# Kernel tuning notes

Measured on AMD Instinct MI355X. Metric: run time of the kernel, lower is better.

The kernel has to match this reference:

```python
import jax, jax.numpy as jnp
import numpy as np

WS = 7          # window size (square)
NUM_HEADS = 4
DIM = 128
B_ = 16384
NW = 64         # number of distinct shift masks


def _relative_coords(ws):
    # [N, N, 2] normalized relative coordinates, N = ws*ws
    ch = jnp.arange(ws, dtype=jnp.float32)
    cw = jnp.arange(ws, dtype=jnp.float32)
    coords = jnp.stack(jnp.meshgrid(ch, cw, indexing='ij'))          # [2, ws, ws]
    flat = coords.reshape(2, -1)                                      # [2, N]
    rel = flat[:, :, None] - flat[:, None, :]                         # [2, N, N]
    rel = jnp.transpose(rel, (1, 2, 0))                               # [N, N, 2]
    denom = jnp.array([max(ws - 1, 1), max(ws - 1, 1)], jnp.float32)
    return rel / denom


def setup_inputs() -> dict:
    key = jax.random.key(0)
    ks = jax.random.split(key, 8)
    N = WS * WS
    return {
        'x': jax.random.normal(ks[0], (B_, N, DIM), jnp.float32),
        'mask': jax.random.normal(ks[1], (NW, N, N), jnp.float32),
        'qkv_w': jax.random.normal(ks[2], (DIM, 3 * DIM), jnp.float32) * 0.02,
        'qkv_b': jnp.zeros((3 * DIM,), jnp.float32),
        'mlp_w1': jax.random.normal(ks[3], (2, 64), jnp.float32) * 0.5,
        'mlp_b1': jnp.zeros((64,), jnp.float32),
        'mlp_w2': jax.random.normal(ks[4], (64, NUM_HEADS), jnp.float32) * 0.1,
        'mlp_b2': jnp.zeros((NUM_HEADS,), jnp.float32),
        'proj_w': jax.random.normal(ks[5], (DIM, DIM), jnp.float32) * 0.02,
        'proj_b': jnp.zeros((DIM,), jnp.float32),
    }


def reference(x, mask, qkv_w, qkv_b, mlp_w1, mlp_b1, mlp_w2, mlp_b2, proj_w, proj_b):
    B, N, C = x.shape
    H = NUM_HEADS
    hd = C // H
    scale = hd ** (-0.5)

    qkv = (x @ qkv_w + qkv_b).reshape(B, N, 3, H, hd)
    qkv = jnp.transpose(qkv, (2, 0, 3, 1, 4))          # [3, B, H, N, hd]
    q, k, v = qkv[0] * scale, qkv[1], qkv[2]

    attn = jnp.einsum('bhnd,bhmd->bhnm', q, k)          # [B, H, N, N]

    # MLP-derived relative position bias (exact-erf GELU, as torch nn.GELU default)
    rel = _relative_coords(WS)                          # [N, N, 2]
    hmid = jax.nn.gelu(rel @ mlp_w1 + mlp_b1, approximate=False)
    bias = hmid @ mlp_w2 + mlp_b2                       # [N, N, H]
    bias = jnp.transpose(bias, (2, 0, 1))               # [H, N, N]
    attn = attn + bias[None]

    nW = mask.shape[0]
    attn = attn.reshape(B // nW, nW, H, N, N) + mask[None, :, None]
    attn = attn.reshape(B, H, N, N)
    attn = jax.nn.softmax(attn, axis=-1)

    out = jnp.einsum('bhnm,bhmd->bhnd', attn, v)        # [B, H, N, hd]
    out = jnp.transpose(out, (0, 2, 1, 3)).reshape(B, N, C)
    return out @ proj_w + proj_b
```

## Files before the change

### kernel.cpp

```cpp
#include <hip/hip_runtime.h>
#include <hip/hip_bf16.h>
#include <math.h>

typedef __bf16 bf16_t;
typedef __bf16 bf16x4 __attribute__((ext_vector_type(4)));
typedef __bf16 bf16x8 __attribute__((ext_vector_type(8)));
typedef float  f32x4  __attribute__((ext_vector_type(4)));

#define QKV_SCALE 0.17677669529663687f

#define WS_QKVWT   0u
#define WS_PROJWT  98304u
#define WS_QKVB    131072u
#define WS_MASKP   135168u
#define WS_BIAST   1183744u

__global__ __launch_bounds__(256) void prep_kernel(
    const float* __restrict__ mask,
    const float* __restrict__ qkv_w, const float* __restrict__ qkv_b,
    const float* __restrict__ mlp_w1, const float* __restrict__ mlp_b1,
    const float* __restrict__ mlp_w2, const float* __restrict__ mlp_b2,
    const float* __restrict__ proj_w,
    bf16_t* __restrict__ qkv_wT, bf16_t* __restrict__ proj_wT,
    float* __restrict__ qkv_bs, float* __restrict__ mask_pad,
    float* __restrict__ bias_t)
{
    const int blk = blockIdx.x;
    const int tid = threadIdx.x;
    if (blk < 1024) {
        const int idx = blk * 256 + tid;
        const int wi = idx >> 12, cell = idx & 4095;
        const int q = cell >> 6, kk = cell & 63;
        float val;
        if (q < 49 && kk < 49)      val = mask[wi * 2401 + q * 49 + kk];
        else if (kk >= 49)          val = -3.0e38f;
        else                        val = 0.0f;
        mask_pad[idx] = val;
    } else if (blk < 1040) {
        const int cell = (blk - 1024) * 256 + tid;
        const int q = cell >> 6, kk = cell & 63;
        float b0 = 0.f, b1 = 0.f, b2 = 0.f, b3 = 0.f;
        if (q < 49 && kk < 49) {
            const float dy = (float)(q / 7 - kk / 7) * (1.0f / 6.0f);
            const float dx = (float)(q % 7 - kk % 7) * (1.0f / 6.0f);
            b0 = mlp_b2[0]; b1 = mlp_b2[1]; b2 = mlp_b2[2]; b3 = mlp_b2[3];
            for (int j = 0; j < 64; ++j) {
                const float pre = dy * mlp_w1[j] + dx * mlp_w1[64 + j] + mlp_b1[j];
                const float g = 0.5f * pre * (1.0f + erff(pre * 0.70710678118654752f));
                b0 += g * mlp_w2[j * 4 + 0];
                b1 += g * mlp_w2[j * 4 + 1];
                b2 += g * mlp_w2[j * 4 + 2];
                b3 += g * mlp_w2[j * 4 + 3];
            }
        }
        bias_t[0 * 4096 + cell] = b0;
        bias_t[1 * 4096 + cell] = b1;
        bias_t[2 * 4096 + cell] = b2;
        bias_t[3 * 4096 + cell] = b3;
    } else if (blk < 1232) {
        const int idx = (blk - 1040) * 256 + tid;
        const int n = idx >> 7, k = idx & 127;
        float v = qkv_w[k * 384 + n];
        if (n < 128) v *= QKV_SCALE;
        qkv_wT[idx] = (bf16_t)v;
    } else if (blk < 1296) {
        const int idx = (blk - 1232) * 256 + tid;
        const int n = idx >> 7, k = idx & 127;
        proj_wT[idx] = (bf16_t)proj_w[k * 128 + n];
    } else {
        if (tid < 384) {
            float v = qkv_b[tid];
            if (tid < 128) v *= QKV_SCALE;
            qkv_bs[tid] = v;
        }
    }
}

__global__ __launch_bounds__(512, 4) void swin_main_kernel(
    const float* __restrict__ x,
    const bf16_t* __restrict__ qkv_wT,
    const bf16_t* __restrict__ proj_wT,
    const float* __restrict__ qkv_bs,
    const float* __restrict__ proj_b,
    const float* __restrict__ mask_pad,
    const float* __restrict__ bias_t,
    float* __restrict__ out)
{
    __shared__ __align__(16) unsigned char smem[65536];
    const int QB = 16384, KBo = 32768, VT = 49152;

    const int win  = blockIdx.x;
    const int tid  = threadIdx.x;
    const int wv   = tid >> 6;
    const int a    = wv >> 1;
    const int b2   = wv & 1;
    const int lane = tid & 63;
    const int c16  = lane & 15;
    const int q4   = lane >> 4;
    const int swz  = (c16 & 7) << 4;
    const f32x4 zf = {0.f, 0.f, 0.f, 0.f};

    {
        const float* xg = x + (size_t)win * 6272;
#pragma unroll
        for (int cc = 0; cc < 2; ++cc) {
            const int c   = tid + 512 * cc;
            const int row = c >> 4;
            const int k8  = (c & 15) << 3;
            const int off = ((row << 8) + (k8 << 1)) ^ ((row & 7) << 4);
            bf16x8 v;
            if (row < 49) {
                const float4 a0 = *(const float4*)(xg + row * 128 + k8);
                const float4 a1 = *(const float4*)(xg + row * 128 + k8 + 4);
                v[0] = (bf16_t)a0.x; v[1] = (bf16_t)a0.y;
                v[2] = (bf16_t)a0.z; v[3] = (bf16_t)a0.w;
                v[4] = (bf16_t)a1.x; v[5] = (bf16_t)a1.y;
                v[6] = (bf16_t)a1.z; v[7] = (bf16_t)a1.w;
            } else {
#pragma unroll
                for (int j = 0; j < 8; ++j) v[j] = (bf16_t)0.0f;
            }
            *(bf16x8*)&smem[off] = v;
        }
    }
    __syncthreads();

    int trow[2];
    trow[0] = (16 * (2 * b2 + 0) + c16) << 8;
    trow[1] = (16 * (2 * b2 + 1) + c16) << 8;

    f32x4 qk[4][2];
#pragma unroll
    for (int m = 0; m < 4; ++m) { qk[m][0] = zf; qk[m][1] = zf; }
#pragma unroll
    for (int ks = 0; ks < 4; ++ks) {
        bf16x8 xf[2];
#pragma unroll
        for (int nt = 0; nt < 2; ++nt)
            xf[nt] = *(const bf16x8*)&smem[(trow[nt] + 64 * ks + 16 * q4) ^ swz];
#pragma unroll
        for (int m = 0; m < 4; ++m) {
            const int t = 4 * a + m;
            const bf16x8 wf = *(const bf16x8*)(qkv_wT + (16 * t + c16) * 128 + ks * 32 + q4 * 8);
#pragma unroll
            for (int nt = 0; nt < 2; ++nt)
                qk[m][nt] = __builtin_amdgcn_mfma_f32_16x16x32_bf16(wf, xf[nt], qk[m][nt], 0, 0, 0);
        }
    }
#pragma unroll
    for (int m = 0; m < 4; ++m) {
        const int t = 4 * a + m;
        const float4 bi = *(const float4*)(qkv_bs + 16 * t + 4 * q4);
        const int base = (t < 8) ? QB : KBo;
        const int dimb = (t < 8) ? (32 * t + 8 * q4) : (32 * (t - 8) + 8 * q4);
#pragma unroll
        for (int nt = 0; nt < 2; ++nt) {
            bf16x4 pk;
            pk[0] = (bf16_t)(qk[m][nt][0] + bi.x); pk[1] = (bf16_t)(qk[m][nt][1] + bi.y);
            pk[2] = (bf16_t)(qk[m][nt][2] + bi.z); pk[3] = (bf16_t)(qk[m][nt][3] + bi.w);
            *(bf16x4*)&smem[base + ((trow[nt] + dimb) ^ swz)] = pk;
        }
    }

    f32x4 va[2][2];
#pragma unroll
    for (int mv = 0; mv < 2; ++mv) { va[mv][0] = zf; va[mv][1] = zf; }
#pragma unroll
    for (int ks = 0; ks < 4; ++ks) {
        bf16x8 xf[2];
#pragma unroll
        for (int nt = 0; nt < 2; ++nt)
            xf[nt] = *(const bf16x8*)&smem[(trow[nt] + 64 * ks + 16 * q4) ^ swz];
#pragma unroll
        for (int mv = 0; mv < 2; ++mv) {
            const int vc = 16 * (2 * a + mv) + c16;
            const bf16x8 vf = *(const bf16x8*)(qkv_wT + (256 + vc) * 128 + ks * 32 + q4 * 8);
#pragma unroll
            for (int nt = 0; nt < 2; ++nt)
                va[mv][nt] = __builtin_amdgcn_mfma_f32_16x16x32_bf16(xf[nt], vf, va[mv][nt], 0, 0, 0);
        }
    }
#pragma unroll
    for (int mv = 0; mv < 2; ++mv) {
        const int vc = 16 * (2 * a + mv) + c16;
        const float qv = qkv_bs[256 + vc];
#pragma unroll
        for (int nt = 0; nt < 2; ++nt) {
            const int slot2 = (32 * b2 + 8 * q4 + 4 * nt) << 1;
            bf16x4 pk;
            pk[0] = (bf16_t)(va[mv][nt][0] + qv); pk[1] = (bf16_t)(va[mv][nt][1] + qv);
            pk[2] = (bf16_t)(va[mv][nt][2] + qv); pk[3] = (bf16_t)(va[mv][nt][3] + qv);
            *(bf16x4*)&smem[VT + (((vc << 7) + slot2) ^ swz)] = pk;
        }
    }
    __syncthreads();

    bf16x8 Qf[2];
#pragma unroll
    for (int nt = 0; nt < 2; ++nt)
        Qf[nt] = *(const bf16x8*)&smem[QB + ((trow[nt] + 64 * a + 16 * q4) ^ swz)];
    f32x4 st[4][2];
#pragma unroll
    for (int mtk = 0; mtk < 4; ++mtk) {
        const bf16x8 Kf = *(const bf16x8*)&smem[KBo + ((((16 * mtk + c16) << 8) + 64 * a + 16 * q4) ^ swz)];
        st[mtk][0] = __builtin_amdgcn_mfma_f32_16x16x32_bf16(Kf, Qf[0], zf, 0, 0, 0);
        st[mtk][1] = __builtin_amdgcn_mfma_f32_16x16x32_bf16(Kf, Qf[1], zf, 0, 0, 0);
    }

    const float* mp = mask_pad + ((size_t)(win & 63) << 12);
    const float* bt = bias_t + (a << 12);
    bf16x8 Pf[2][2];
#pragma unroll
    for (int ntq = 0; ntq < 2; ++ntq) {
        const int qtok = 16 * (2 * b2 + ntq) + c16;
        float mx = -3.0e38f;
#pragma unroll
        for (int mtk = 0; mtk < 4; ++mtk) {
            const float4 mv4 = *(const float4*)(mp + qtok * 64 + 16 * mtk + 4 * q4);
            const float4 bv4 = *(const float4*)(bt + qtok * 64 + 16 * mtk + 4 * q4);
            st[mtk][ntq][0] += mv4.x + bv4.x; st[mtk][ntq][1] += mv4.y + bv4.y;
            st[mtk][ntq][2] += mv4.z + bv4.z; st[mtk][ntq][3] += mv4.w + bv4.w;
#pragma unroll
            for (int r = 0; r < 4; ++r) mx = fmaxf(mx, st[mtk][ntq][r]);
        }
        mx = fmaxf(mx, __shfl_xor(mx, 16));
        mx = fmaxf(mx, __shfl_xor(mx, 32));
        float sm = 0.0f;
#pragma unroll
        for (int mtk = 0; mtk < 4; ++mtk)
#pragma unroll
            for (int r = 0; r < 4; ++r) {
                const float p = __expf(st[mtk][ntq][r] - mx);
                st[mtk][ntq][r] = p;
                sm += p;
            }
        sm += __shfl_xor(sm, 16);
        sm += __shfl_xor(sm, 32);
        const float rp = 1.0f / sm;
#pragma unroll
        for (int ksv = 0; ksv < 2; ++ksv)
#pragma unroll
            for (int r = 0; r < 4; ++r) {
                Pf[ntq][ksv][r]     = (bf16_t)(st[2 * ksv][ntq][r] * rp);
                Pf[ntq][ksv][4 + r] = (bf16_t)(st[2 * ksv + 1][ntq][r] * rp);
            }
    }

    f32x4 ot[2][2];
#pragma unroll
    for (int mtd = 0; mtd < 2; ++mtd) { ot[mtd][0] = zf; ot[mtd][1] = zf; }
#pragma unroll
    for (int ksv = 0; ksv < 2; ++ksv)
#pragma unroll
        for (int mtd = 0; mtd < 2; ++mtd) {
            const bf16x8 av = *(const bf16x8*)&smem[VT + ((((32 * a + 16 * mtd + c16) << 7) + 64 * ksv + 16 * q4) ^ swz)];
#pragma unroll
            for (int ntq = 0; ntq < 2; ++ntq)
                ot[mtd][ntq] = __builtin_amdgcn_mfma_f32_16x16x32_bf16(av, Pf[ntq][ksv], ot[mtd][ntq], 0, 0, 0);
        }

#pragma unroll
    for (int mtd = 0; mtd < 2; ++mtd)
#pragma unroll
        for (int ntq = 0; ntq < 2; ++ntq) {
            bf16x4 pk;
#pragma unroll
            for (int r = 0; r < 4; ++r) pk[r] = (bf16_t)ot[mtd][ntq][r];
            *(bf16x4*)&smem[(trow[ntq] + ((32 * a + 16 * mtd + 4 * q4) << 1)) ^ swz] = pk;
        }
    __syncthreads();

    const int oc_il = 32 * a + 8 * (c16 >> 2) + (c16 & 3);
    f32x4 pj[2][2];
#pragma unroll
    for (int mt = 0; mt < 2; ++mt) { pj[mt][0] = zf; pj[mt][1] = zf; }
#pragma unroll
    for (int ks = 0; ks < 4; ++ks) {
        const bf16x8 aw0 = *(const bf16x8*)(proj_wT + (oc_il + 0) * 128 + ks * 32 + q4 * 8);
        const bf16x8 aw1 = *(const bf16x8*)(proj_wT + (oc_il + 4) * 128 + ks * 32 + q4 * 8);
#pragma unroll
        for (int ntq = 0; ntq < 2; ++ntq) {
            const bf16x8 bo = *(const bf16x8*)&smem[(trow[ntq] + 64 * ks + 16 * q4) ^ swz];
            pj[0][ntq] = __builtin_amdgcn_mfma_f32_16x16x32_bf16(aw0, bo, pj[0][ntq], 0, 0, 0);
            pj[1][ntq] = __builtin_amdgcn_mfma_f32_16x16x32_bf16(aw1, bo, pj[1][ntq], 0, 0, 0);
        }
    }

    {
        float* og = out + (size_t)win * 6272;
        const int oc0 = 32 * a + 8 * q4;
        const float4 pb0 = *(const float4*)(proj_b + oc0);
        const float4 pb1 = *(const float4*)(proj_b + oc0 + 4);
#pragma unroll
        for (int ntq = 0; ntq < 2; ++ntq) {
            const int tok = 16 * (2 * b2 + ntq) + c16;
            if (tok < 49) {
                float4 v0, v1;
                v0.x = pj[0][ntq][0] + pb0.x; v0.y = pj[0][ntq][1] + pb0.y;
                v0.z = pj[0][ntq][2] + pb0.z; v0.w = pj[0][ntq][3] + pb0.w;
                v1.x = pj[1][ntq][0] + pb1.x; v1.y = pj[1][ntq][1] + pb1.y;
                v1.z = pj[1][ntq][2] + pb1.z; v1.w = pj[1][ntq][3] + pb1.w;
                *(float4*)(og + tok * 128 + oc0)     = v0;
                *(float4*)(og + tok * 128 + oc0 + 4) = v1;
            }
        }
    }
}

extern "C" void kernel_launch(void* const* d_in, const int* in_sizes, int n_in,
                              void* d_out, int out_size, void* d_ws, size_t ws_size,
                              hipStream_t stream) {
    const float* x      = (const float*)d_in[0];
    const float* mask   = (const float*)d_in[1];
    const float* qkv_w  = (const float*)d_in[2];
    const float* qkv_b  = (const float*)d_in[3];
    const float* mlp_w1 = (const float*)d_in[4];
    const float* mlp_b1 = (const float*)d_in[5];
    const float* mlp_w2 = (const float*)d_in[6];
    const float* mlp_b2 = (const float*)d_in[7];
    const float* proj_w = (const float*)d_in[8];
    const float* proj_b = (const float*)d_in[9];
    float* out = (float*)d_out;

    unsigned char* ws = (unsigned char*)d_ws;
    bf16_t* qkv_wT   = (bf16_t*)(ws + WS_QKVWT);
    bf16_t* proj_wT  = (bf16_t*)(ws + WS_PROJWT);
    float*  qkv_bs   = (float*)(ws + WS_QKVB);
    float*  mask_pad = (float*)(ws + WS_MASKP);
    float*  bias_t   = (float*)(ws + WS_BIAST);

    hipLaunchKernelGGL(prep_kernel, dim3(1297), dim3(256), 0, stream,
                       mask, qkv_w, qkv_b, mlp_w1, mlp_b1, mlp_w2, mlp_b2, proj_w,
                       qkv_wT, proj_wT, qkv_bs, mask_pad, bias_t);
    hipLaunchKernelGGL(swin_main_kernel, dim3(16384), dim3(512), 0, stream,
                       x, qkv_wT, proj_wT, qkv_bs, proj_b, mask_pad, bias_t, out);
}
```

Before: 795.8 us.

## Process eight windows per block with double-buffered x prefetch

Each block now loops over several consecutive windows instead of one. While the current window is computed, the next window's x tile is loaded from global memory into registers and written into a second LDS buffer, which overlaps load latency with compute. Per-block constants such as biases are hoisted out of the loop. In exchange, LDS use grows to 80KB, occupancy drops to 2 blocks, the grid shrinks by 8x, and an extra barrier is added per window.

```diff
diff --git a/kernel.cpp b/kernel.cpp
--- a/kernel.cpp
+++ b/kernel.cpp
@@ -8,6 +8,7 @@
 typedef float  f32x4  __attribute__((ext_vector_type(4)));
 
 #define QKV_SCALE 0.17677669529663687f
+#define NWIN 8
 
 #define WS_QKVWT   0u
 #define WS_PROJWT  98304u
@@ -76,7 +77,7 @@
     }
 }
 
-__global__ __launch_bounds__(512, 4) void swin_main_kernel(
+__global__ __launch_bounds__(512, 2) void swin_main_kernel(
     const float* __restrict__ x,
     const bf16_t* __restrict__ qkv_wT,
     const bf16_t* __restrict__ proj_wT,
@@ -86,10 +87,9 @@
     const float* __restrict__ bias_t,
     float* __restrict__ out)
 {
-    __shared__ __align__(16) unsigned char smem[65536];
-    const int QB = 16384, KBo = 32768, VT = 49152;
-
-    const int win  = blockIdx.x;
+    __shared__ __align__(16) unsigned char smem[81920];
+    const int QB = 32768, KBo = 49152, VT = 65536;
+
     const int tid  = threadIdx.x;
     const int wv   = tid >> 6;
     const int a    = wv >> 1;
@@ -98,20 +98,43 @@
     const int c16  = lane & 15;
     const int q4   = lane >> 4;
     const int swz  = (c16 & 7) << 4;
+    const int wbase = blockIdx.x * NWIN;
     const f32x4 zf = {0.f, 0.f, 0.f, 0.f};
 
+    float4 biQK[4];
+#pragma unroll
+    for (int m = 0; m < 4; ++m)
+        biQK[m] = *(const float4*)(qkv_bs + 16 * (4 * a + m) + 4 * q4);
+    float qv[2];
+    qv[0] = qkv_bs[256 + 16 * (2 * a + 0) + c16];
+    qv[1] = qkv_bs[256 + 16 * (2 * a + 1) + c16];
+    const int oc_il = 32 * a + 8 * (c16 >> 2) + (c16 & 3);
+    const int oc0   = 32 * a + 8 * q4;
+    const float4 pb0 = *(const float4*)(proj_b + oc0);
+    const float4 pb1 = *(const float4*)(proj_b + oc0 + 4);
+    const float* bt = bias_t + (a << 12);
+
+    int trow[2];
+    trow[0] = (16 * (2 * b2 + 0) + c16) << 8;
+    trow[1] = (16 * (2 * b2 + 1) + c16) << 8;
+
+    int srow[2], sk8[2], soff[2];
+#pragma unroll
+    for (int cc = 0; cc < 2; ++cc) {
+        const int c = tid + 512 * cc;
+        srow[cc] = c >> 4;
+        sk8[cc]  = (c & 15) << 3;
+        soff[cc] = ((srow[cc] << 8) + (sk8[cc] << 1)) ^ ((srow[cc] & 7) << 4);
+    }
+
     {
-        const float* xg = x + (size_t)win * 6272;
+        const float* xg = x + (size_t)wbase * 6272;
 #pragma unroll
         for (int cc = 0; cc < 2; ++cc) {
-            const int c   = tid + 512 * cc;
-            const int row = c >> 4;
-            const int k8  = (c & 15) << 3;
-            const int off = ((row << 8) + (k8 << 1)) ^ ((row & 7) << 4);
             bf16x8 v;
-            if (row < 49) {
-                const float4 a0 = *(const float4*)(xg + row * 128 + k8);
-                const float4 a1 = *(const float4*)(xg + row * 128 + k8 + 4);
+            if (srow[cc] < 49) {
+                const float4 a0 = *(const float4*)(xg + srow[cc] * 128 + sk8[cc]);
+                const float4 a1 = *(const float4*)(xg + srow[cc] * 128 + sk8[cc] + 4);
                 v[0] = (bf16_t)a0.x; v[1] = (bf16_t)a0.y;
                 v[2] = (bf16_t)a0.z; v[3] = (bf16_t)a0.w;
                 v[4] = (bf16_t)a1.x; v[5] = (bf16_t)a1.y;
@@ -120,190 +143,216 @@
 #pragma unroll
                 for (int j = 0; j < 8; ++j) v[j] = (bf16_t)0.0f;
             }
-            *(bf16x8*)&smem[off] = v;
+            *(bf16x8*)&smem[soff[cc]] = v;
         }
     }
     __syncthreads();
 
-    int trow[2];
-    trow[0] = (16 * (2 * b2 + 0) + c16) << 8;
-    trow[1] = (16 * (2 * b2 + 1) + c16) << 8;
-
-    f32x4 qk[4][2];
-#pragma unroll
-    for (int m = 0; m < 4; ++m) { qk[m][0] = zf; qk[m][1] = zf; }
-#pragma unroll
-    for (int ks = 0; ks < 4; ++ks) {
-        bf16x8 xf[2];
-#pragma unroll
-        for (int nt = 0; nt < 2; ++nt)
-            xf[nt] = *(const bf16x8*)&smem[(trow[nt] + 64 * ks + 16 * q4) ^ swz];
+    for (int i = 0; i < NWIN; ++i) {
+        const int win  = wbase + i;
+        const int xcur = (i & 1) << 14;
+        const int xnxt = ((i & 1) ^ 1) << 14;
+        const bool pf  = (i + 1 < NWIN);
+
+        float4 pa[2][2];
+        if (pf) {
+            const float* xn = x + (size_t)(win + 1) * 6272;
+#pragma unroll
+            for (int cc = 0; cc < 2; ++cc) {
+                if (srow[cc] < 49) {
+                    pa[cc][0] = *(const float4*)(xn + srow[cc] * 128 + sk8[cc]);
+                    pa[cc][1] = *(const float4*)(xn + srow[cc] * 128 + sk8[cc] + 4);
+                }
+            }
+        }
+
+        f32x4 qk[4][2];
+#pragma unroll
+        for (int m = 0; m < 4; ++m) { qk[m][0] = zf; qk[m][1] = zf; }
+#pragma unroll
+        for (int ks = 0; ks < 4; ++ks) {
+            bf16x8 xf[2];
+#pragma unroll
+            for (int nt = 0; nt < 2; ++nt)
+                xf[nt] = *(const bf16x8*)&smem[xcur + ((trow[nt] + 64 * ks + 16 * q4) ^ swz)];
+#pragma unroll
+            for (int m = 0; m < 4; ++m) {
+                const int t = 4 * a + m;
+                const bf16x8 wf = *(const bf16x8*)(qkv_wT + (16 * t + c16) * 128 + ks * 32 + q4 * 8);
+#pragma unroll
+                for (int nt = 0; nt < 2; ++nt)
+                    qk[m][nt] = __builtin_amdgcn_mfma_f32_16x16x32_bf16(wf, xf[nt], qk[m][nt], 0, 0, 0);
+            }
+        }
 #pragma unroll
         for (int m = 0; m < 4; ++m) {
             const int t = 4 * a + m;
-            const bf16x8 wf = *(const bf16x8*)(qkv_wT + (16 * t + c16) * 128 + ks * 32 + q4 * 8);
+            const int base = (t < 8) ? QB : KBo;
+            const int dimb = (t < 8) ? (32 * t + 8 * q4) : (32 * (t - 8) + 8 * q4);
+#pragma unroll
+            for (int nt = 0; nt < 2; ++nt) {
+                bf16x4 pk;
+                pk[0] = (bf16_t)(qk[m][nt][0] + biQK[m].x); pk[1] = (bf16_t)(qk[m][nt][1] + biQK[m].y);
+                pk[2] = (bf16_t)(qk[m][nt][2] + biQK[m].z); pk[3] = (bf16_t)(qk[m][nt][3] + biQK[m].w);
+                *(bf16x4*)&smem[base + ((trow[nt] + dimb) ^ swz)] = pk;
+            }
+        }
+
+        f32x4 va[2][2];
+#pragma unroll
+        for (int mv = 0; mv < 2; ++mv) { va[mv][0] = zf; va[mv][1] = zf; }
+#pragma unroll
+        for (int ks = 0; ks < 4; ++ks) {
+            bf16x8 xf[2];
 #pragma unroll
             for (int nt = 0; nt < 2; ++nt)
-                qk[m][nt] = __builtin_amdgcn_mfma_f32_16x16x32_bf16(wf, xf[nt], qk[m][nt], 0, 0, 0);
-        }
-    }
-#pragma unroll
-    for (int m = 0; m < 4; ++m) {
-        const int t = 4 * a + m;
-        const float4 bi = *(const float4*)(qkv_bs + 16 * t + 4 * q4);
-        const int base = (t < 8) ? QB : KBo;
-        const int dimb = (t < 8) ? (32 * t + 8 * q4) : (32 * (t - 8) + 8 * q4);
-#pragma unroll
-        for (int nt = 0; nt < 2; ++nt) {
-            bf16x4 pk;
-            pk[0] = (bf16_t)(qk[m][nt][0] + bi.x); pk[1] = (bf16_t)(qk[m][nt][1] + bi.y);
-            pk[2] = (bf16_t)(qk[m][nt][2] + bi.z); pk[3] = (bf16_t)(qk[m][nt][3] + bi.w);
-            *(bf16x4*)&smem[base + ((trow[nt] + dimb) ^ swz)] = pk;
-        }
-    }
-
-    f32x4 va[2][2];
-#pragma unroll
-    for (int mv = 0; mv < 2; ++mv) { va[mv][0] = zf; va[mv][1] = zf; }
-#pragma unroll
-    for (int ks = 0; ks < 4; ++ks) {
-        bf16x8 xf[2];
-#pragma unroll
-        for (int nt = 0; nt < 2; ++nt)
-            xf[nt] = *(const bf16x8*)&smem[(trow[nt] + 64 * ks + 16 * q4) ^ swz];
+                xf[nt] = *(const bf16x8*)&smem[xcur + ((trow[nt] + 64 * ks + 16 * q4) ^ swz)];
+#pragma unroll
+            for (int mv = 0; mv < 2; ++mv) {
+                const int vc = 16 * (2 * a + mv) + c16;
+                const bf16x8 vf = *(const bf16x8*)(qkv_wT + (256 + vc) * 128 + ks * 32 + q4 * 8);
+#pragma unroll
+                for (int nt = 0; nt < 2; ++nt)
+                    va[mv][nt] = __builtin_amdgcn_mfma_f32_16x16x32_bf16(xf[nt], vf, va[mv][nt], 0, 0, 0);
+            }
+        }
 #pragma unroll
         for (int mv = 0; mv < 2; ++mv) {
             const int vc = 16 * (2 * a + mv) + c16;
-            const bf16x8 vf = *(const bf16x8*)(qkv_wT + (256 + vc) * 128 + ks * 32 + q4 * 8);
-#pragma unroll
-            for (int nt = 0; nt < 2; ++nt)
-                va[mv][nt] = __builtin_amdgcn_mfma_f32_16x16x32_bf16(xf[nt], vf, va[mv][nt], 0, 0, 0);
-        }
-    }
-#pragma unroll
-    for (int mv = 0; mv < 2; ++mv) {
-        const int vc = 16 * (2 * a + mv) + c16;
-        const float qv = qkv_bs[256 + vc];
-#pragma unroll
-        for (int nt = 0; nt < 2; ++nt) {
-            const int slot2 = (32 * b2 + 8 * q4 + 4 * nt) << 1;
-            bf16x4 pk;
-            pk[0] = (bf16_t)(va[mv][nt][0] + qv); pk[1] = (bf16_t)(va[mv][nt][1] + qv);
-            pk[2] = (bf16_t)(va[mv][nt][2] + qv); pk[3] = (bf16_t)(va[mv][nt][3] + qv);
-            *(bf16x4*)&smem[VT + (((vc << 7) + slot2) ^ swz)] = pk;
-        }
-    }
-    __syncthreads();
-
-    bf16x8 Qf[2];
-#pragma unroll
-    for (int nt = 0; nt < 2; ++nt)
-        Qf[nt] = *(const bf16x8*)&smem[QB + ((trow[nt] + 64 * a + 16 * q4) ^ swz)];
-    f32x4 st[4][2];
-#pragma unroll
-    for (int mtk = 0; mtk < 4; ++mtk) {
-        const bf16x8 Kf = *(const bf16x8*)&smem[KBo + ((((16 * mtk + c16) << 8) + 64 * a + 16 * q4) ^ swz)];
-        st[mtk][0] = __builtin_amdgcn_mfma_f32_16x16x32_bf16(Kf, Qf[0], zf, 0, 0, 0);
-        st[mtk][1] = __builtin_amdgcn_mfma_f32_16x16x32_bf16(Kf, Qf[1], zf, 0, 0, 0);
-    }
-
-    const float* mp = mask_pad + ((size_t)(win & 63) << 12);
-    const float* bt = bias_t + (a << 12);
-    bf16x8 Pf[2][2];
-#pragma unroll
-    for (int ntq = 0; ntq < 2; ++ntq) {
-        const int qtok = 16 * (2 * b2 + ntq) + c16;
-        float mx = -3.0e38f;
+#pragma unroll
+            for (int nt = 0; nt < 2; ++nt) {
+                const int slot2 = (32 * b2 + 8 * q4 + 4 * nt) << 1;
+                bf16x4 pk;
+                pk[0] = (bf16_t)(va[mv][nt][0] + qv[mv]); pk[1] = (bf16_t)(va[mv][nt][1] + qv[mv]);
+                pk[2] = (bf16_t)(va[mv][nt][2] + qv[mv]); pk[3] = (bf16_t)(va[mv][nt][3] + qv[mv]);
+                *(bf16x4*)&smem[VT + (((vc << 7) + slot2) ^ swz)] = pk;
+            }
+        }
+
+        if (pf) {
+#pragma unroll
+            for (int cc = 0; cc < 2; ++cc) {
+                bf16x8 v;
+                if (srow[cc] < 49) {
+                    v[0] = (bf16_t)pa[cc][0].x; v[1] = (bf16_t)pa[cc][0].y;
+                    v[2] = (bf16_t)pa[cc][0].z; v[3] = (bf16_t)pa[cc][0].w;
+                    v[4] = (bf16_t)pa[cc][1].x; v[5] = (bf16_t)pa[cc][1].y;
+                    v[6] = (bf16_t)pa[cc][1].z; v[7] = (bf16_t)pa[cc][1].w;
+                } else {
+#pragma unroll
+                    for (int j = 0; j < 8; ++j) v[j] = (bf16_t)0.0f;
+                }
+                *(bf16x8*)&smem[xnxt + soff[cc]] = v;
+            }
+        }
+        __syncthreads();
+
+        bf16x8 Qf[2];
+#pragma unroll
+        for (int nt = 0; nt < 2; ++nt)
+            Qf[nt] = *(const bf16x8*)&smem[QB + ((trow[nt] + 64 * a + 16 * q4) ^ swz)];
+        f32x4 st[4][2];
 #pragma unroll
         for (int mtk = 0; mtk < 4; ++mtk) {
-            const float4 mv4 = *(const float4*)(mp + qtok * 64 + 16 * mtk + 4 * q4);
-            const float4 bv4 = *(const float4*)(bt + qtok * 64 + 16 * mtk + 4 * q4);
-            st[mtk][ntq][0] += mv4.x + bv4.x; st[mtk][ntq][1] += mv4.y + bv4.y;
-            st[mtk][ntq][2] += mv4.z + bv4.z; st[mtk][ntq][3] += mv4.w + bv4.w;
-#pragma unroll
-            for (int r = 0; r < 4; ++r) mx = fmaxf(mx, st[mtk][ntq][r]);
-        }
-        mx = fmaxf(mx, __shfl_xor(mx, 16));
-        mx = fmaxf(mx, __shfl_xor(mx, 32));
-        float sm = 0.0f;
-#pragma unroll
-        for (int mtk = 0; mtk < 4; ++mtk)
-#pragma unroll
-            for (int r = 0; r < 4; ++r) {
-                const float p = __expf(st[mtk][ntq][r] - mx);
-                st[mtk][ntq][r] = p;
-                sm += p;
-            }
-        sm += __shfl_xor(sm, 16);
-        sm += __shfl_xor(sm, 32);
-        const float rp = 1.0f / sm;
+            const bf16x8 Kf = *(const bf16x8*)&smem[KBo + ((((16 * mtk + c16) << 8) + 64 * a + 16 * q4) ^ swz)];
+            st[mtk][0] = __builtin_amdgcn_mfma_f32_16x16x32_bf16(Kf, Qf[0], zf, 0, 0, 0);
+            st[mtk][1] = __builtin_amdgcn_mfma_f32_16x16x32_bf16(Kf, Qf[1], zf, 0, 0, 0);
+        }
+
+        const float* mp = mask_pad + ((size_t)(win & 63) << 12);
+        bf16x8 Pf[2][2];
+#pragma unroll
+        for (int ntq = 0; ntq < 2; ++ntq) {
+            const int qtok = 16 * (2 * b2 + ntq) + c16;
+            float mx = -3.0e38f;
+#pragma unroll
+            for (int mtk = 0; mtk < 4; ++mtk) {
+                const float4 mv4 = *(const float4*)(mp + qtok * 64 + 16 * mtk + 4 * q4);
+                const float4 bv4 = *(const float4*)(bt + qtok * 64 + 16 * mtk + 4 * q4);
+                st[mtk][ntq][0] += mv4.x + bv4.x; st[mtk][ntq][1] += mv4.y + bv4.y;
+                st[mtk][ntq][2] += mv4.z + bv4.z; st[mtk][ntq][3] += mv4.w + bv4.w;
+#pragma unroll
+                for (int r = 0; r < 4; ++r) mx = fmaxf(mx, st[mtk][ntq][r]);
+            }
+            mx = fmaxf(mx, __shfl_xor(mx, 16));
+            mx = fmaxf(mx, __shfl_xor(mx, 32));
+            float sm = 0.0f;
+#pragma unroll
+            for (int mtk = 0; mtk < 4; ++mtk)
+#pragma unroll
+                for (int r = 0; r < 4; ++r) {
+                    const float p = __expf(st[mtk][ntq][r] - mx);
+                    st[mtk][ntq][r] = p;
+                    sm += p;
+                }
+            sm += __shfl_xor(sm, 16);
+            sm += __shfl_xor(sm, 32);
+            const float rp = 1.0f / sm;
+#pragma unroll
+            for (int ksv = 0; ksv < 2; ++ksv)
+#pragma unroll
+                for (int r = 0; r < 4; ++r) {
+                    Pf[ntq][ksv][r]     = (bf16_t)(st[2 * ksv][ntq][r] * rp);
+                    Pf[ntq][ksv][4 + r] = (bf16_t)(st[2 * ksv + 1][ntq][r] * rp);
+                }
+        }
+
+        f32x4 ot[2][2];
+#pragma unroll
+        for (int mtd = 0; mtd < 2; ++mtd) { ot[mtd][0] = zf; ot[mtd][1] = zf; }
 #pragma unroll
         for (int ksv = 0; ksv < 2; ++ksv)
 #pragma unroll
-            for (int r = 0; r < 4; ++r) {
-                Pf[ntq][ksv][r]     = (bf16_t)(st[2 * ksv][ntq][r] * rp);
-                Pf[ntq][ksv][4 + r] = (bf16_t)(st[2 * ksv + 1][ntq][r] * rp);
-            }
-    }
-
-    f32x4 ot[2][2];
-#pragma unroll
-    for (int mtd = 0; mtd < 2; ++mtd) { ot[mtd][0] = zf; ot[mtd][1] = zf; }
-#pragma unroll
-    for (int ksv = 0; ksv < 2; ++ksv)
-#pragma unroll
-        for (int mtd = 0; mtd < 2; ++mtd) {
-            const bf16x8 av = *(const bf16x8*)&smem[VT + ((((32 * a + 16 * mtd + c16) << 7) + 64 * ksv + 16 * q4) ^ swz)];
-#pragma unroll
-            for (int ntq = 0; ntq < 2; ++ntq)
-                ot[mtd][ntq] = __builtin_amdgcn_mfma_f32_16x16x32_bf16(av, Pf[ntq][ksv], ot[mtd][ntq], 0, 0, 0);
-        }
-
-#pragma unroll
-    for (int mtd = 0; mtd < 2; ++mtd)
-#pragma unroll
-        for (int ntq = 0; ntq < 2; ++ntq) {
-            bf16x4 pk;
-#pragma unroll
-            for (int r = 0; r < 4; ++r) pk[r] = (bf16_t)ot[mtd][ntq][r];
-            *(bf16x4*)&smem[(trow[ntq] + ((32 * a + 16 * mtd + 4 * q4) << 1)) ^ swz] = pk;
-        }
-    __syncthreads();
-
-    const int oc_il = 32 * a + 8 * (c16 >> 2) + (c16 & 3);
-    f32x4 pj[2][2];
-#pragma unroll
-    for (int mt = 0; mt < 2; ++mt) { pj[mt][0] = zf; pj[mt][1] = zf; }
-#pragma unroll
-    for (int ks = 0; ks < 4; ++ks) {
-        const bf16x8 aw0 = *(const bf16x8*)(proj_wT + (oc_il + 0) * 128 + ks * 32 + q4 * 8);
-        const bf16x8 aw1 = *(const bf16x8*)(proj_wT + (oc_il + 4) * 128 + ks * 32 + q4 * 8);
-#pragma unroll
-        for (int ntq = 0; ntq < 2; ++ntq) {
-            const bf16x8 bo = *(const bf16x8*)&smem[(trow[ntq] + 64 * ks + 16 * q4) ^ swz];
-            pj[0][ntq] = __builtin_amdgcn_mfma_f32_16x16x32_bf16(aw0, bo, pj[0][ntq], 0, 0, 0);
-            pj[1][ntq] = __builtin_amdgcn_mfma_f32_16x16x32_bf16(aw1, bo, pj[1][ntq], 0, 0, 0);
-        }
-    }
-
-    {
-        float* og = out + (size_t)win * 6272;
-        const int oc0 = 32 * a + 8 * q4;
-        const float4 pb0 = *(const float4*)(proj_b + oc0);
-        const float4 pb1 = *(const float4*)(proj_b + oc0 + 4);
-#pragma unroll
-        for (int ntq = 0; ntq < 2; ++ntq) {
-            const int tok = 16 * (2 * b2 + ntq) + c16;
-            if (tok < 49) {
-                float4 v0, v1;
-                v0.x = pj[0][ntq][0] + pb0.x; v0.y = pj[0][ntq][1] + pb0.y;
-                v0.z = pj[0][ntq][2] + pb0.z; v0.w = pj[0][ntq][3] + pb0.w;
-                v1.x = pj[1][ntq][0] + pb1.x; v1.y = pj[1][ntq][1] + pb1.y;
-                v1.z = pj[1][ntq][2] + pb1.z; v1.w = pj[1][ntq][3] + pb1.w;
-                *(float4*)(og + tok * 128 + oc0)     = v0;
-                *(float4*)(og + tok * 128 + oc0 + 4) = v1;
-            }
-        }
+            for (int mtd = 0; mtd < 2; ++mtd) {
+                const bf16x8 av = *(const bf16x8*)&smem[VT + ((((32 * a + 16 * mtd + c16) << 7) + 64 * ksv + 16 * q4) ^ swz)];
+#pragma unroll
+                for (int ntq = 0; ntq < 2; ++ntq)
+                    ot[mtd][ntq] = __builtin_amdgcn_mfma_f32_16x16x32_bf16(av, Pf[ntq][ksv], ot[mtd][ntq], 0, 0, 0);
+            }
+
+#pragma unroll
+        for (int mtd = 0; mtd < 2; ++mtd)
+#pragma unroll
+            for (int ntq = 0; ntq < 2; ++ntq) {
+                bf16x4 pk;
+#pragma unroll
+                for (int r = 0; r < 4; ++r) pk[r] = (bf16_t)ot[mtd][ntq][r];
+                *(bf16x4*)&smem[xcur + ((trow[ntq] + ((32 * a + 16 * mtd + 4 * q4) << 1)) ^ swz)] = pk;
+            }
+        __syncthreads();
+
+        f32x4 pj[2][2];
+#pragma unroll
+        for (int mt = 0; mt < 2; ++mt) { pj[mt][0] = zf; pj[mt][1] = zf; }
+#pragma unroll
+        for (int ks = 0; ks < 4; ++ks) {
+            const bf16x8 aw0 = *(const bf16x8*)(proj_wT + (oc_il + 0) * 128 + ks * 32 + q4 * 8);
+            const bf16x8 aw1 = *(const bf16x8*)(proj_wT + (oc_il + 4) * 128 + ks * 32 + q4 * 8);
+#pragma unroll
+            for (int ntq = 0; ntq < 2; ++ntq) {
+                const bf16x8 bo = *(const bf16x8*)&smem[xcur + ((trow[ntq] + 64 * ks + 16 * q4) ^ swz)];
+                pj[0][ntq] = __builtin_amdgcn_mfma_f32_16x16x32_bf16(aw0, bo, pj[0][ntq], 0, 0, 0);
+                pj[1][ntq] = __builtin_amdgcn_mfma_f32_16x16x32_bf16(aw1, bo, pj[1][ntq], 0, 0, 0);
+            }
+        }
+
+        {
+            float* og = out + (size_t)win * 6272;
+#pragma unroll
+            for (int ntq = 0; ntq < 2; ++ntq) {
+                const int tok = 16 * (2 * b2 + ntq) + c16;
+                if (tok < 49) {
+                    float4 v0, v1;
+                    v0.x = pj[0][ntq][0] + pb0.x; v0.y = pj[0][ntq][1] + pb0.y;
+                    v0.z = pj[0][ntq][2] + pb0.z; v0.w = pj[0][ntq][3] + pb0.w;
+                    v1.x = pj[1][ntq][0] + pb1.x; v1.y = pj[1][ntq][1] + pb1.y;
+                    v1.z = pj[1][ntq][2] + pb1.z; v1.w = pj[1][ntq][3] + pb1.w;
+                    *(float4*)(og + tok * 128 + oc0)     = v0;
+                    *(float4*)(og + tok * 128 + oc0 + 4) = v1;
+                }
+            }
+        }
+        __syncthreads();
     }
 }
 
@@ -332,6 +381,6 @@
     hipLaunchKernelGGL(prep_kernel, dim3(1297), dim3(256), 0, stream,
                        mask, qkv_w, qkv_b, mlp_w1, mlp_b1, mlp_w2, mlp_b2, proj_w,
                        qkv_wT, proj_wT, qkv_bs, mask_pad, bias_t);
-    hipLaunchKernelGGL(swin_main_kernel, dim3(16384), dim3(512), 0, stream,
+    hipLaunchKernelGGL(swin_main_kernel, dim3(16384 / NWIN), dim3(512), 0, stream,
                        x, qkv_wT, proj_wT, qkv_bs, proj_b, mask_pad, bias_t, out);
 }
```

Measured after the change: 1.084 ms. 36.3% more time.
